# Optimization experiments

Measured on AMD Instinct MI355X. Metric: run time of the kernel, lower is better.

Reference implementation:

```python
import jax, jax.numpy as jnp
import numpy as np

EPS = 1e-12  # torch F.normalize clamp_min eps


def _linear_interp(t, M):
    # PyTorch F.interpolate(mode='linear', align_corners=False) along last axis.
    L = t.shape[-1]
    src = (jnp.arange(M, dtype=t.dtype) + 0.5) * (L / M) - 0.5
    src = jnp.maximum(src, 0.0)
    i0 = jnp.minimum(jnp.floor(src).astype(jnp.int32), L - 1)
    i1 = jnp.minimum(i0 + 1, L - 1)
    frac = src - i0.astype(t.dtype)
    return t[..., i0] * (1.0 - frac) + t[..., i1] * frac


def _l2norm(t):
    n = jnp.linalg.norm(t, axis=-1, keepdims=True)
    return t / jnp.maximum(n, EPS)


def setup_inputs() -> dict:
    key = jax.random.key(0)
    ks = jax.random.split(key, 6)
    b, dim, m = 4, 512, 4096
    h = w = 64
    heads = 8
    s = 0.02
    return {
        "x": jax.random.normal(ks[0], (b, dim, m), dtype=jnp.float32),
        "y": jax.random.normal(ks[1], (b, dim, h, w), dtype=jnp.float32),
        "temperature": jnp.ones((heads, 1, 1), dtype=jnp.float32),
        "w_kv": jax.random.normal(ks[2], (2 * dim, dim), dtype=jnp.float32) * s,
        "w_q": jax.random.normal(ks[3], (dim, dim), dtype=jnp.float32) * s,
        "w_dw": jax.random.normal(ks[4], (dim, dim, 3, 3), dtype=jnp.float32) * s,
        "w_out": jax.random.normal(ks[5], (dim, dim), dtype=jnp.float32) * s,
    }


def reference(x, y, temperature, w_kv, w_q, w_dw, w_out):
    b, c, m = x.shape
    heads = temperature.shape[0]
    hd = c // heads

    # kv = Conv1d(dim, 2*dim, k=1)(x); split into k, v
    kv = jnp.einsum('bcm,oc->bom', x, w_kv)
    k, v = jnp.split(kv, 2, axis=1)

    # q = dwconv3x3(Conv2d 1x1(y)) -> flatten -> linear-resize to m
    q = jnp.einsum('bchw,oc->bohw', y, w_q)
    q = jax.lax.conv_general_dilated(
        q, w_dw, window_strides=(1, 1), padding=[(1, 1), (1, 1)],
        dimension_numbers=('NCHW', 'OIHW', 'NCHW'))
    q = q.reshape(b, c, -1)
    q = _linear_interp(q, m)

    # split heads: [b, head, c', m]
    q = _l2norm(q.reshape(b, heads, hd, m))
    k = _l2norm(k.reshape(b, heads, hd, m))
    v = v.reshape(b, heads, hd, m)

    # channel-wise attention: [b, head, c', c']
    attn = jnp.einsum('bhcm,bhdm->bhcd', q, k) * temperature
    attn = jax.nn.softmax(attn, axis=-1)
    out = jnp.einsum('bhcd,bhdm->bhcm', attn, v).reshape(b, c, m)

    # project_out: Conv1d k=1
    return jnp.einsum('bcm,oc->bom', out, w_out)
```

## Files before the change

### kernel.cpp

```cpp
#include <hip/hip_runtime.h>
#include <hip/hip_bf16.h>
#include <math.h>

typedef float f32x4 __attribute__((ext_vector_type(4)));
typedef int   i32x4 __attribute__((ext_vector_type(4)));
typedef short s16x8 __attribute__((ext_vector_type(8)));

#define NB 4
#define NC 512
#define NM 4096
#define NHEADS 8

#define GLDS16(src, dst) __builtin_amdgcn_global_load_lds( \
    (const __attribute__((address_space(1))) void*)(src),  \
    (__attribute__((address_space(3))) void*)(dst), 16, 0, 0)

__global__ __launch_bounds__(256) void prep(
    const float* __restrict__ wdw, const float* __restrict__ wkv,
    const float* __restrict__ wq,
    __hip_bfloat16* __restrict__ Wr, __hip_bfloat16* __restrict__ wkvB,
    __hip_bfloat16* __restrict__ wqT, __hip_bfloat16* __restrict__ zeropad,
    float* __restrict__ norms)
{
  long idx = (long)blockIdx.x * 256 + threadIdx.x;
  if (idx < 2359296) {
    int r = (int)(idx / 262144);
    int rem = (int)(idx % 262144);
    int o = rem >> 9, i = rem & 511;
    Wr[idx] = __float2bfloat16(wdw[((long)o * 512 + i) * 9 + r]);
  } else if (idx < 2883584) {
    long j = idx - 2359296;
    wkvB[j] = __float2bfloat16(wkv[j]);
  } else if (idx < 3145728) {
    long j = idx - 2883584;
    int c = (int)(j >> 9), cp = (int)(j & 511);
    wqT[j] = __float2bfloat16(wq[(long)cp * 512 + c]);
  } else if (idx < 3145856) {
    zeropad[idx - 3145728] = __float2bfloat16(0.f);
  } else if (idx < 3149952) {
    norms[idx - 3145856] = 0.f;
  }
}

__global__ __launch_bounds__(256) void transpose_k(
    const float* __restrict__ x, const float* __restrict__ y,
    __hip_bfloat16* __restrict__ xT, __hip_bfloat16* __restrict__ yT)
{
  __shared__ __hip_bfloat16 tile[64][68];
  int z = blockIdx.z;
  const float* src = ((z < 4) ? x : y) + (long)(z & 3) * ((long)NC * NM);
  __hip_bfloat16* dst = (z < 4 ? xT : yT) + (long)(z & 3) * ((long)NC * NM);
  int tm = blockIdx.x * 64, tc = blockIdx.y * 64;
  int tx4 = threadIdx.x & 15, trow = threadIdx.x >> 4;
  #pragma unroll
  for (int p = 0; p < 4; p++) {
    int crow = trow + p * 16;
    f32x4 v = *(const f32x4*)&src[(long)(tc + crow) * NM + tm + tx4 * 4];
    #pragma unroll
    for (int t = 0; t < 4; t++) tile[crow][tx4 * 4 + t] = __float2bfloat16(v[t]);
  }
  __syncthreads();
  #pragma unroll
  for (int p = 0; p < 4; p++) {
    int mrow = trow + p * 16;
    union { ushort4 u4; unsigned short u[4]; } o;
    #pragma unroll
    for (int t = 0; t < 4; t++)
      o.u[t] = *(const unsigned short*)&tile[tx4 * 4 + t][mrow];
    *(ushort4*)&dst[(long)(tm + mrow) * NC + tc + tx4 * 4] = o.u4;
  }
}

__global__ __launch_bounds__(256) void gemm_bt(
    const __hip_bfloat16* __restrict__ Aall, long sA,
    const __hip_bfloat16* __restrict__ Ball, long sB,
    __hip_bfloat16* __restrict__ Cball, float* __restrict__ Cfall, long sC,
    int M, int N, int Kd, int outMode)
{
  const __hip_bfloat16* A = Aall + (long)blockIdx.z * sA;
  const __hip_bfloat16* B = Ball + (long)blockIdx.z * sB;
  const int m0 = blockIdx.y * 128, n0 = blockIdx.x * 128;
  __shared__ __hip_bfloat16 As[128 * 32];
  __shared__ __hip_bfloat16 Bs[128 * 32];
  const int tid = threadIdx.x;
  const int wid = tid >> 6, lane = tid & 63;
  const int wm = (wid >> 1) * 64, wn = (wid & 1) * 64;
  const int quad = lane >> 4, l16 = lane & 15;
  const int srow = wid * 32 + (lane >> 2);
  const int scol = (lane & 3) * 8;
  f32x4 acc[4][4] = {};
  for (int k0 = 0; k0 < Kd; k0 += 32) {
    __syncthreads();
    #pragma unroll
    for (int t = 0; t < 2; t++) {
      GLDS16(A + (long)(m0 + srow + t * 16) * Kd + k0 + scol,
             As + (wid * 32 + t * 16) * 32);
      GLDS16(B + (long)(n0 + srow + t * 16) * Kd + k0 + scol,
             Bs + (wid * 32 + t * 16) * 32);
    }
    __builtin_amdgcn_s_waitcnt(0);
    __syncthreads();
    s16x8 bfr[4];
    #pragma unroll
    for (int j = 0; j < 4; j++)
      bfr[j] = *(const s16x8*)(&Bs[(wn + j * 16 + l16) * 32 + quad * 8]);
    #pragma unroll
    for (int i = 0; i < 4; i++) {
      s16x8 af = *(const s16x8*)(&As[(wm + i * 16 + l16) * 32 + quad * 8]);
      #pragma unroll
      for (int j = 0; j < 4; j++)
        acc[i][j] = __builtin_amdgcn_mfma_f32_16x16x32_bf16(af, bfr[j], acc[i][j], 0, 0, 0);
    }
  }
  if (outMode == 1) {
    float* C = Cfall + (long)blockIdx.z * sC;
    #pragma unroll
    for (int i = 0; i < 4; i++)
      #pragma unroll
      for (int j = 0; j < 4; j++) {
        int rbase = m0 + wm + i * 16 + quad * 4;
        int col = n0 + wn + j * 16 + l16;
        #pragma unroll
        for (int r = 0; r < 4; r++)
          C[(long)(rbase + r) * N + col] = acc[i][j][r];
      }
  } else if (outMode == 2) {
    __hip_bfloat16* C = Cball;
    const int rt = blockIdx.z;
    #pragma unroll
    for (int i = 0; i < 4; i++)
      #pragma unroll
      for (int j = 0; j < 4; j++) {
        int obase = m0 + wm + i * 16 + quad * 4;
        int col = n0 + wn + j * 16 + l16;
        #pragma unroll
        for (int r = 0; r < 4; r++) {
          int o = obase + r;
          long idx = ((((long)(rt * 32 + (o >> 4)) * 16 + (col >> 5)) << 9)
                      + ((col >> 3) & 3) * 128 + (o & 15) * 8 + (col & 7));
          C[idx] = __float2bfloat16(acc[i][j][r]);
        }
      }
  } else {
    __hip_bfloat16* C = Cball + (long)blockIdx.z * sC;
    #pragma unroll
    for (int i = 0; i < 4; i++)
      #pragma unroll
      for (int j = 0; j < 4; j++) {
        int rbase = m0 + wm + i * 16 + quad * 4;
        int col = n0 + wn + j * 16 + l16;
        #pragma unroll
        for (int r = 0; r < 4; r++)
          C[(long)(rbase + r) * N + col] = __float2bfloat16(acc[i][j][r]);
      }
  }
}

__global__ __launch_bounds__(256) void gemm_kv(
    const __hip_bfloat16* __restrict__ wkvB,
    const __hip_bfloat16* __restrict__ xT,
    __hip_bfloat16* __restrict__ Kb,
    __hip_bfloat16* __restrict__ Vt,
    float* __restrict__ knorm2)
{
  const int z = blockIdx.z;
  const int b = z & 3;
  const bool kmode = (z < 4);
  const long S = (long)NM * NC;
  const __hip_bfloat16* A = kmode ? wkvB : (xT + b * S);
  const __hip_bfloat16* B = kmode ? (xT + b * S) : (wkvB + 262144);
  __hip_bfloat16* C = kmode ? (Kb + b * S) : (Vt + b * S);
  const int m0 = (kmode ? blockIdx.y : blockIdx.x) * 128;
  const int n0 = (kmode ? blockIdx.x : blockIdx.y) * 128;
  const int N = kmode ? NM : NC;
  __shared__ __hip_bfloat16 As[128 * 32];
  __shared__ __hip_bfloat16 Bs[128 * 32];
  const int tid = threadIdx.x;
  const int wid = tid >> 6, lane = tid & 63;
  const int wm = (wid >> 1) * 64, wn = (wid & 1) * 64;
  const int quad = lane >> 4, l16 = lane & 15;
  const int srow = wid * 32 + (lane >> 2);
  const int scol = (lane & 3) * 8;
  f32x4 acc[4][4] = {};
  for (int k0 = 0; k0 < NC; k0 += 32) {
    __syncthreads();
    #pragma unroll
    for (int t = 0; t < 2; t++) {
      GLDS16(A + (long)(m0 + srow + t * 16) * NC + k0 + scol,
             As + (wid * 32 + t * 16) * 32);
      GLDS16(B + (long)(n0 + srow + t * 16) * NC + k0 + scol,
             Bs + (wid * 32 + t * 16) * 32);
    }
    __builtin_amdgcn_s_waitcnt(0);
    __syncthreads();
    s16x8 bfr[4];
    #pragma unroll
    for (int j = 0; j < 4; j++)
      bfr[j] = *(const s16x8*)(&Bs[(wn + j * 16 + l16) * 32 + quad * 8]);
    #pragma unroll
    for (int i = 0; i < 4; i++) {
      s16x8 af = *(const s16x8*)(&As[(wm + i * 16 + l16) * 32 + quad * 8]);
      #pragma unroll
      for (int j = 0; j < 4; j++)
        acc[i][j] = __builtin_amdgcn_mfma_f32_16x16x32_bf16(af, bfr[j], acc[i][j], 0, 0, 0);
    }
  }
  #pragma unroll
  for (int i = 0; i < 4; i++)
    #pragma unroll
    for (int j = 0; j < 4; j++) {
      int rbase = m0 + wm + i * 16 + quad * 4;
      int col = n0 + wn + j * 16 + l16;
      #pragma unroll
      for (int r = 0; r < 4; r++)
        C[(long)(rbase + r) * N + col] = __float2bfloat16(acc[i][j][r]);
    }
  if (kmode) {
    #pragma unroll
    for (int i = 0; i < 4; i++) {
      int rbase = m0 + wm + i * 16 + quad * 4;
      #pragma unroll
      for (int r = 0; r < 4; r++) {
        float s = 0.f;
        #pragma unroll
        for (int j = 0; j < 4; j++) s += acc[i][j][r] * acc[i][j][r];
        s += __shfl_xor(s, 1); s += __shfl_xor(s, 2);
        s += __shfl_xor(s, 4); s += __shfl_xor(s, 8);
        if (l16 == 0) atomicAdd(&knorm2[b * 512 + rbase + r], s);
      }
    }
  }
}

__global__ __launch_bounds__(256) void conv3x3(
    const __hip_bfloat16* __restrict__ Wp,
    const __hip_bfloat16* __restrict__ yT,
    const __hip_bfloat16* __restrict__ zeropad,
    __hip_bfloat16* __restrict__ q2,
    float* __restrict__ qnorm2)
{
  const int b = blockIdx.z;
  const int n0 = blockIdx.x * 128;
  const int m0 = blockIdx.y * 128;
  __shared__ __hip_bfloat16 Bs[256 * 32];
  const int tid = threadIdx.x;
  const int wid = tid >> 6, lane = tid & 63;
  const int wm = (wid >> 1) * 64, wn = (wid & 1) * 64;
  const int quad = lane >> 4, l16 = lane & 15;
  const int lrow = lane >> 2;
  const int h0 = n0 >> 6;
  const __hip_bfloat16* yb = yT + (long)b * NM * NC;
  f32x4 acc[4][4] = {};
  const s16x8 zero8 = {0, 0, 0, 0, 0, 0, 0, 0};

  const int sq = ((lane & 3) ^ ((lane >> 3) & 3)) * 8;

  const int mb0 = (m0 + wm) >> 4;
  const __hip_bfloat16* Abase = Wp + (long)lane * 8;

  int addr0[3][4];
  unsigned vbits = 0;
  #pragma unroll
  for (int t = 0; t < 3; t++) {
    #pragma unroll
    for (int j = 0; j < 4; j++) {
      int nl = wn + j * 16 + l16;
      int wq_ = nl & 63, hr = nl >> 6;
      int wp = wq_ + t - 1;
      unsigned v = ((unsigned)wp) < 64u;
      int p = v ? (hr * 64 + wp) : 0;
      addr0[t][j] = p * 32 + ((quad ^ ((p >> 1) & 3)) * 8);
      vbits |= v << (t * 4 + j);
    }
  }

  for (int icb = 0; icb < 16; icb++) {
    __syncthreads();
    #pragma unroll
    for (int t = 0; t < 4; t++) {
      int p = wid * 64 + t * 16 + lrow;
      int hw = (h0 - 1) * 64 + p;
      const __hip_bfloat16* src = (((unsigned)hw) < (unsigned)NM)
          ? (yb + (long)hw * NC + icb * 32 + sq) : zeropad;
      GLDS16(src, Bs + (wid * 64 + t * 16) * 32);
    }
    __builtin_amdgcn_s_waitcnt(0);
    __syncthreads();
    #pragma unroll
    for (int g = 0; g < 3; g++) {
      #pragma unroll
      for (int t = 0; t < 3; t++) {
        const int rt = g * 3 + t;
        s16x8 bfr[4];
        #pragma unroll
        for (int j = 0; j < 4; j++) {
          s16x8 tt = *(const s16x8*)(&Bs[addr0[t][j] + g * 2048]);
          bfr[j] = ((vbits >> (t * 4 + j)) & 1u) ? tt : zero8;
        }
        #pragma unroll
        for (int i = 0; i < 4; i++) {
          s16x8 af = *(const s16x8*)(Abase +
              ((long)((rt * 32 + mb0 + i) * 16 + icb) << 9));
          #pragma unroll
          for (int j = 0; j < 4; j++)
            acc[i][j] = __builtin_amdgcn_mfma_f32_16x16x32_bf16(af, bfr[j], acc[i][j], 0, 0, 0);
        }
      }
    }
  }
  __hip_bfloat16* Cb = q2 + (long)b * NC * NM;
  #pragma unroll
  for (int i = 0; i < 4; i++)
    #pragma unroll
    for (int j = 0; j < 4; j++) {
      int rbase = m0 + wm + i * 16 + quad * 4;
      int col = n0 + wn + j * 16 + l16;
      #pragma unroll
      for (int r = 0; r < 4; r++)
        Cb[(long)(rbase + r) * NM + col] = __float2bfloat16(acc[i][j][r]);
    }
  #pragma unroll
  for (int i = 0; i < 4; i++) {
    int rbase = m0 + wm + i * 16 + quad * 4;
    #pragma unroll
    for (int r = 0; r < 4; r++) {
      float s = 0.f;
      #pragma unroll
      for (int j = 0; j < 4; j++) s += acc[i][j][r] * acc[i][j][r];
      s += __shfl_xor(s, 1); s += __shfl_xor(s, 2);
      s += __shfl_xor(s, 4); s += __shfl_xor(s, 8);
      if (l16 == 0) atomicAdd(&qnorm2[b * 512 + rbase + r], s);
    }
  }
}

__global__ __launch_bounds__(256) void attn_g(
    const __hip_bfloat16* __restrict__ q2, const __hip_bfloat16* __restrict__ Kb,
    float* __restrict__ Gpart)
{
  const int mc = blockIdx.x, h = blockIdx.y, b = blockIdx.z;
  const __hip_bfloat16* qrow = q2 + ((long)b * NC + h * 64) * NM + mc * 512;
  const __hip_bfloat16* krow = Kb + ((long)b * NC + h * 64) * NM + mc * 512;
  __shared__ __hip_bfloat16 Qs[64 * 40];
  __shared__ __hip_bfloat16 Ks[64 * 40];
  const int tid = threadIdx.x;
  const int wid = tid >> 6, lane = tid & 63;
  const int wc = (wid >> 1) * 32, wd = (wid & 1) * 32;
  const int quad = lane >> 4, l16 = lane & 15;
  const int srow = tid >> 2, scol = (tid & 3) * 8;
  f32x4 acc[2][2] = {};
  for (int k0 = 0; k0 < 512; k0 += 32) {
    __syncthreads();
    *(i32x4*)(&Qs[srow * 40 + scol]) = *(const i32x4*)(&qrow[(long)srow * NM + k0 + scol]);
    *(i32x4*)(&Ks[srow * 40 + scol]) = *(const i32x4*)(&krow[(long)srow * NM + k0 + scol]);
    __syncthreads();
    s16x8 bfr[2];
    #pragma unroll
    for (int j = 0; j < 2; j++)
      bfr[j] = *(const s16x8*)(&Ks[(wd + j * 16 + l16) * 40 + quad * 8]);
    #pragma unroll
    for (int i = 0; i < 2; i++) {
      s16x8 af = *(const s16x8*)(&Qs[(wc + i * 16 + l16) * 40 + quad * 8]);
      #pragma unroll
      for (int j = 0; j < 2; j++)
        acc[i][j] = __builtin_amdgcn_mfma_f32_16x16x32_bf16(af, bfr[j], acc[i][j], 0, 0, 0);
    }
  }
  float* gp = Gpart + ((long)((b * 8 + h) * 8 + mc)) * 4096;
  #pragma unroll
  for (int i = 0; i < 2; i++)
    #pragma unroll
    for (int j = 0; j < 2; j++)
      #pragma unroll
      for (int r = 0; r < 4; r++)
        gp[(wc + i * 16 + quad * 4 + r) * 64 + wd + j * 16 + l16] = acc[i][j][r];
}

__global__ __launch_bounds__(256) void softmax_wa(
    const float* __restrict__ Gpart, const float* __restrict__ qnorm2,
    const float* __restrict__ knorm2, const float* __restrict__ temp,
    const float* __restrict__ wout, __hip_bfloat16* __restrict__ Wa)
{
  const int oc = blockIdx.x, h = blockIdx.y, b = blockIdx.z;
  __shared__ float G[64][64];
  __shared__ float Wt[64][65];
  const int tid = threadIdx.x;
  const float tv = temp[h];
  for (int e = tid; e < 4096; e += 256) {
    float s = 0.f;
    #pragma unroll
    for (int p = 0; p < 8; p++)
      s += Gpart[((long)((b * 8 + h) * 8 + p)) * 4096 + e];
    int c = e >> 6, d = e & 63;
    float qn = fmaxf(sqrtf(qnorm2[b * 512 + h * 64 + c]), 1e-12f);
    float kn = fmaxf(sqrtf(knorm2[b * 512 + h * 64 + d]), 1e-12f);
    G[c][d] = s * tv / (qn * kn);
    Wt[c][d] = wout[(long)(oc * 64 + c) * 512 + h * 64 + d];
  }
  __syncthreads();
  int row = tid >> 2, s4 = tid & 3;
  float mx = -1e30f;
  for (int d = s4; d < 64; d += 4) mx = fmaxf(mx, G[row][d]);
  mx = fmaxf(mx, __shfl_xor(mx, 1));
  mx = fmaxf(mx, __shfl_xor(mx, 2));
  float sum = 0.f;
  for (int d = s4; d < 64; d += 4) { float e = __expf(G[row][d] - mx); G[row][d] = e; sum += e; }
  sum += __shfl_xor(sum, 1);
  sum += __shfl_xor(sum, 2);
  float inv = 1.f / sum;
  for (int d = s4; d < 64; d += 4) G[row][d] *= inv;
  __syncthreads();
  int d = tid & 63, og = tid >> 6;
  #pragma unroll
  for (int k2 = 0; k2 < 16; k2++) {
    int o = og * 16 + k2;
    float s = 0.f;
    #pragma unroll 8
    for (int c = 0; c < 64; c++) s += Wt[o][c] * G[c][d];
    Wa[((long)b * 512 + oc * 64 + o) * 512 + h * 64 + d] = __float2bfloat16(s);
  }
}

extern "C" void kernel_launch(void* const* d_in, const int* in_sizes, int n_in,
                              void* d_out, int out_size, void* d_ws, size_t ws_size,
                              hipStream_t stream) {
  const float* x    = (const float*)d_in[0];
  const float* y    = (const float*)d_in[1];
  const float* temp = (const float*)d_in[2];
  const float* wkv  = (const float*)d_in[3];
  const float* wq   = (const float*)d_in[4];
  const float* wdw  = (const float*)d_in[5];
  const float* wout = (const float*)d_in[6];
  float* out = (float*)d_out;

  char* ws = (char*)d_ws;
  const long TEN = 16777216;
  __hip_bfloat16* xT  = (__hip_bfloat16*)(ws);
  __hip_bfloat16* q2  = xT;
  __hip_bfloat16* yT  = (__hip_bfloat16*)(ws + TEN);
  float* Gpart        = (float*)(ws + TEN);
  __hip_bfloat16* Wa  = (__hip_bfloat16*)(ws + TEN + 4718592);
  __hip_bfloat16* Kb  = (__hip_bfloat16*)(ws + 2 * TEN);
  __hip_bfloat16* Vt  = (__hip_bfloat16*)(ws + 3 * TEN);
  __hip_bfloat16* Wfold = (__hip_bfloat16*)(ws + 4 * TEN);
  __hip_bfloat16* Wr    = (__hip_bfloat16*)(ws + 4 * TEN + 4718592);
  __hip_bfloat16* wkvB  = (__hip_bfloat16*)(ws + 4 * TEN + 9437184);
  __hip_bfloat16* wqT   = (__hip_bfloat16*)(ws + 4 * TEN + 10485760);
  __hip_bfloat16* zeropad = (__hip_bfloat16*)(ws + 4 * TEN + 11010048);
  float* norms          = (float*)(ws + 4 * TEN + 11010304);
  float* knorm2 = norms;
  float* qnorm2 = norms + 2048;

  const long S = (long)4096 * 512;
  const long S2 = (long)512 * 512;
  dim3 blk(256);

  prep<<<dim3(12305), blk, 0, stream>>>(wdw, wkv, wq, Wr, wkvB, wqT, zeropad, norms);
  transpose_k<<<dim3(64, 8, 8), blk, 0, stream>>>(x, y, xT, yT);
  gemm_bt<<<dim3(4, 4, 9), blk, 0, stream>>>(Wr, S2, wqT, 0L, Wfold, nullptr, 0L, 512, 512, 512, 2);
  gemm_kv<<<dim3(32, 4, 8), blk, 0, stream>>>(wkvB, xT, Kb, Vt, knorm2);
  conv3x3<<<dim3(32, 4, 4), blk, 0, stream>>>(Wfold, yT, zeropad, q2, qnorm2);
  attn_g<<<dim3(8, 8, 4), blk, 0, stream>>>(q2, Kb, Gpart);
  softmax_wa<<<dim3(8, 8, 4), blk, 0, stream>>>(Gpart, qnorm2, knorm2, temp, wout, Wa);
  gemm_bt<<<dim3(32, 4, 4), blk, 0, stream>>>(Wa, S2, Vt, S, nullptr, out, S, 512, 4096, 512, 1);
  (void)in_sizes; (void)n_in; (void)out_size; (void)ws_size;
}
```

Before: 323.0 us.

## Double-buffer conv3x3 weight and input tiles in LDS with async prefetch

The 3x3 conv GEMM kernel now stages the weight (A) fragments through LDS instead of reading them directly from global memory on every MFMA step. Both the A and B tiles are double-buffered, and the next stage is prefetched with global_load_lds while the current stage computes. This is meant to hide global load latency and cut redundant global weight reads across waves. In exchange it uses much more LDS (about 80KB per block), which may lower occupancy, and adds a barrier per tap group.

```diff
diff --git a/kernel.cpp b/kernel.cpp
--- a/kernel.cpp
+++ b/kernel.cpp
@@ -242,21 +242,21 @@
   const int b = blockIdx.z;
   const int n0 = blockIdx.x * 128;
   const int m0 = blockIdx.y * 128;
-  __shared__ __hip_bfloat16 Bs[256 * 32];
+  __shared__ __hip_bfloat16 As2[2][24 * 512];
+  __shared__ __hip_bfloat16 Bs2[2][256 * 32];
   const int tid = threadIdx.x;
   const int wid = tid >> 6, lane = tid & 63;
   const int wm = (wid >> 1) * 64, wn = (wid & 1) * 64;
   const int quad = lane >> 4, l16 = lane & 15;
   const int lrow = lane >> 2;
   const int h0 = n0 >> 6;
+  const int mb0b = m0 >> 4;
+  const int mwl = wm >> 4;
   const __hip_bfloat16* yb = yT + (long)b * NM * NC;
   f32x4 acc[4][4] = {};
   const s16x8 zero8 = {0, 0, 0, 0, 0, 0, 0, 0};
 
   const int sq = ((lane & 3) ^ ((lane >> 3) & 3)) * 8;
-
-  const int mb0 = (m0 + wm) >> 4;
-  const __hip_bfloat16* Abase = Wp + (long)lane * 8;
 
   int addr0[3][4];
   unsigned vbits = 0;
@@ -274,40 +274,73 @@
     }
   }
 
+
+  #pragma unroll
+  for (int k = 0; k < 6; k++) {
+    int f = wid * 6 + k;
+    GLDS16(Wp + (((long)(((f >> 3)) * 32 + mb0b + (f & 7)) * 16 + 0) << 9) + lane * 8,
+           &As2[0][f * 512]);
+  }
+  #pragma unroll
+  for (int t = 0; t < 4; t++) {
+    int pr = wid * 64 + t * 16 + lrow;
+    int hw = (h0 - 1) * 64 + pr;
+    const __hip_bfloat16* src = (((unsigned)hw) < (unsigned)NM)
+        ? (yb + (long)hw * NC + sq) : zeropad;
+    GLDS16(src, &Bs2[0][(wid * 64 + t * 16) * 32]);
+  }
+  __builtin_amdgcn_s_waitcnt(0);
+  __syncthreads();
+
   for (int icb = 0; icb < 16; icb++) {
-    __syncthreads();
-    #pragma unroll
-    for (int t = 0; t < 4; t++) {
-      int p = wid * 64 + t * 16 + lrow;
-      int hw = (h0 - 1) * 64 + p;
-      const __hip_bfloat16* src = (((unsigned)hw) < (unsigned)NM)
-          ? (yb + (long)hw * NC + icb * 32 + sq) : zeropad;
-      GLDS16(src, Bs + (wid * 64 + t * 16) * 32);
-    }
-    __builtin_amdgcn_s_waitcnt(0);
-    __syncthreads();
+    const __hip_bfloat16* Bcur = &Bs2[icb & 1][0];
     #pragma unroll
     for (int g = 0; g < 3; g++) {
+      const int cb = (icb ^ g) & 1;
+      const __hip_bfloat16* Acur = &As2[cb][0];
+      __hip_bfloat16* Anxt = (__hip_bfloat16*)&As2[cb ^ 1][0];
+      if (icb < 15 || g < 2) {
+        const int gn = (g == 2) ? 0 : g + 1;
+        const int icbn = (g == 2) ? icb + 1 : icb;
+        #pragma unroll
+        for (int k = 0; k < 6; k++) {
+          int f = wid * 6 + k;
+          GLDS16(Wp + (((long)((gn * 3 + (f >> 3)) * 32 + mb0b + (f & 7)) * 16 + icbn) << 9) + lane * 8,
+                 Anxt + f * 512);
+        }
+      }
+      if (g == 1 && icb < 15) {
+        __hip_bfloat16* Bnxt = (__hip_bfloat16*)&Bs2[(icb & 1) ^ 1][0];
+        #pragma unroll
+        for (int t = 0; t < 4; t++) {
+          int pr = wid * 64 + t * 16 + lrow;
+          int hw = (h0 - 1) * 64 + pr;
+          const __hip_bfloat16* src = (((unsigned)hw) < (unsigned)NM)
+              ? (yb + (long)hw * NC + (icb + 1) * 32 + sq) : zeropad;
+          GLDS16(src, Bnxt + (wid * 64 + t * 16) * 32);
+        }
+      }
       #pragma unroll
       for (int t = 0; t < 3; t++) {
-        const int rt = g * 3 + t;
         s16x8 bfr[4];
         #pragma unroll
         for (int j = 0; j < 4; j++) {
-          s16x8 tt = *(const s16x8*)(&Bs[addr0[t][j] + g * 2048]);
+          s16x8 tt = *(const s16x8*)(&Bcur[addr0[t][j] + g * 2048]);
           bfr[j] = ((vbits >> (t * 4 + j)) & 1u) ? tt : zero8;
         }
         #pragma unroll
         for (int i = 0; i < 4; i++) {
-          s16x8 af = *(const s16x8*)(Abase +
-              ((long)((rt * 32 + mb0 + i) * 16 + icb) << 9));
+          s16x8 af = *(const s16x8*)(&Acur[(t * 8 + mwl + i) * 512 + lane * 8]);
           #pragma unroll
           for (int j = 0; j < 4; j++)
             acc[i][j] = __builtin_amdgcn_mfma_f32_16x16x32_bf16(af, bfr[j], acc[i][j], 0, 0, 0);
         }
       }
-    }
-  }
+      __builtin_amdgcn_s_waitcnt(0);
+      __syncthreads();
+    }
+  }
+
   __hip_bfloat16* Cb = q2 + (long)b * NC * NM;
   #pragma unroll
   for (int i = 0; i < 4; i++)
```

New measurement: 300.4 us. -7.0%, faster.

## Double-buffer conv3x3 LDS tiles and software-pipeline weight fragment loads

Applied to the files above, without the earlier changes.

The 3x3 conv implicit-GEMM kernel now uses two LDS buffers for the y tiles. The next input-channel block is staged asynchronously while the current one is being consumed. Weight (A) fragments are prefetched one tap ahead into alternating register sets, so global load latency overlaps with the MFMAs. This removes one barrier per iteration and exposes load latency to overlap, at the cost of double the LDS and extra registers, which may reduce occupancy.

```diff
diff --git a/kernel.cpp b/kernel.cpp
--- a/kernel.cpp
+++ b/kernel.cpp
@@ -242,21 +242,21 @@
   const int b = blockIdx.z;
   const int n0 = blockIdx.x * 128;
   const int m0 = blockIdx.y * 128;
-  __shared__ __hip_bfloat16 Bs[256 * 32];
+  __shared__ __hip_bfloat16 Bs2[2][256 * 32];
   const int tid = threadIdx.x;
   const int wid = tid >> 6, lane = tid & 63;
   const int wm = (wid >> 1) * 64, wn = (wid & 1) * 64;
   const int quad = lane >> 4, l16 = lane & 15;
   const int lrow = lane >> 2;
   const int h0 = n0 >> 6;
+  const int mb0b = m0 >> 4;
+  const int mwl = wm >> 4;
   const __hip_bfloat16* yb = yT + (long)b * NM * NC;
+  const __hip_bfloat16* Ab = Wp + (long)lane * 8;
   f32x4 acc[4][4] = {};
   const s16x8 zero8 = {0, 0, 0, 0, 0, 0, 0, 0};
 
   const int sq = ((lane & 3) ^ ((lane >> 3) & 3)) * 8;
-
-  const int mb0 = (m0 + wm) >> 4;
-  const __hip_bfloat16* Abase = Wp + (long)lane * 8;
 
   int addr0[3][4];
   unsigned vbits = 0;
@@ -274,40 +274,81 @@
     }
   }
 
-  for (int icb = 0; icb < 16; icb++) {
-    __syncthreads();
-    #pragma unroll
-    for (int t = 0; t < 4; t++) {
-      int p = wid * 64 + t * 16 + lrow;
-      int hw = (h0 - 1) * 64 + p;
-      const __hip_bfloat16* src = (((unsigned)hw) < (unsigned)NM)
-          ? (yb + (long)hw * NC + icb * 32 + sq) : zeropad;
-      GLDS16(src, Bs + (wid * 64 + t * 16) * 32);
-    }
-    __builtin_amdgcn_s_waitcnt(0);
-    __syncthreads();
-    #pragma unroll
-    for (int g = 0; g < 3; g++) {
-      #pragma unroll
-      for (int t = 0; t < 3; t++) {
-        const int rt = g * 3 + t;
-        s16x8 bfr[4];
-        #pragma unroll
-        for (int j = 0; j < 4; j++) {
-          s16x8 tt = *(const s16x8*)(&Bs[addr0[t][j] + g * 2048]);
-          bfr[j] = ((vbits >> (t * 4 + j)) & 1u) ? tt : zero8;
-        }
-        #pragma unroll
-        for (int i = 0; i < 4; i++) {
-          s16x8 af = *(const s16x8*)(Abase +
-              ((long)((rt * 32 + mb0 + i) * 16 + icb) << 9));
-          #pragma unroll
-          for (int j = 0; j < 4; j++)
-            acc[i][j] = __builtin_amdgcn_mfma_f32_16x16x32_bf16(af, bfr[j], acc[i][j], 0, 0, 0);
-        }
-      }
-    }
-  }
+  s16x8 pA0[4], pA1[4];
+
+#define LOADA(buf, icb_, rt_) { \
+  _Pragma("unroll") \
+  for (int i_ = 0; i_ < 4; i_++) \
+    buf[i_] = *(const s16x8*)(Ab + (((long)((rt_) * 32 + mb0b + mwl + i_) * 16 + (icb_)) << 9)); }
+
+#define TAPC(bufc, g_, t_) { \
+  s16x8 bfr[4]; \
+  _Pragma("unroll") \
+  for (int j_ = 0; j_ < 4; j_++) { \
+    s16x8 tt = *(const s16x8*)(&Bcur[addr0[t_][j_] + (g_) * 2048]); \
+    bfr[j_] = ((vbits >> ((t_) * 4 + j_)) & 1u) ? tt : zero8; \
+  } \
+  _Pragma("unroll") \
+  for (int i_ = 0; i_ < 4; i_++) { \
+    _Pragma("unroll") \
+    for (int j_ = 0; j_ < 4; j_++) \
+      acc[i_][j_] = __builtin_amdgcn_mfma_f32_16x16x32_bf16(bufc[i_], bfr[j_], acc[i_][j_], 0, 0, 0); \
+  } }
+
+#define STAGEB(icb_, bufidx) { \
+  _Pragma("unroll") \
+  for (int t_ = 0; t_ < 4; t_++) { \
+    int pr = wid * 64 + t_ * 16 + lrow; \
+    int hw = (h0 - 1) * 64 + pr; \
+    const __hip_bfloat16* src = (((unsigned)hw) < (unsigned)NM) \
+        ? (yb + (long)hw * NC + (icb_) * 32 + sq) : zeropad; \
+    GLDS16(src, &Bs2[bufidx][(wid * 64 + t_ * 16) * 32]); \
+  } }
+
+  STAGEB(0, 0);
+  LOADA(pA0, 0, 0);
+  __builtin_amdgcn_s_waitcnt(0);
+  __syncthreads();
+
+  for (int i2 = 0; i2 < 8; i2++) {
+    const int icb = 2 * i2;
+    {
+      const __hip_bfloat16* Bcur = &Bs2[0][0];
+      STAGEB(icb + 1, 1);
+      LOADA(pA1, icb, 1);      TAPC(pA0, 0, 0);
+      LOADA(pA0, icb, 2);      TAPC(pA1, 0, 1);
+      LOADA(pA1, icb, 3);      TAPC(pA0, 0, 2);
+      LOADA(pA0, icb, 4);      TAPC(pA1, 1, 0);
+      LOADA(pA1, icb, 5);      TAPC(pA0, 1, 1);
+      LOADA(pA0, icb, 6);      TAPC(pA1, 1, 2);
+      LOADA(pA1, icb, 7);      TAPC(pA0, 2, 0);
+      LOADA(pA0, icb, 8);      TAPC(pA1, 2, 1);
+      LOADA(pA1, icb + 1, 0);  TAPC(pA0, 2, 2);
+      __builtin_amdgcn_s_waitcnt(0);
+      __syncthreads();
+    }
+    {
+      const int icbo = icb + 1;
+      const __hip_bfloat16* Bcur = &Bs2[1][0];
+      if (icbo < 15) STAGEB(icbo + 1, 0);
+      LOADA(pA0, icbo, 1);     TAPC(pA1, 0, 0);
+      LOADA(pA1, icbo, 2);     TAPC(pA0, 0, 1);
+      LOADA(pA0, icbo, 3);     TAPC(pA1, 0, 2);
+      LOADA(pA1, icbo, 4);     TAPC(pA0, 1, 0);
+      LOADA(pA0, icbo, 5);     TAPC(pA1, 1, 1);
+      LOADA(pA1, icbo, 6);     TAPC(pA0, 1, 2);
+      LOADA(pA0, icbo, 7);     TAPC(pA1, 2, 0);
+      LOADA(pA1, icbo, 8);     TAPC(pA0, 2, 1);
+      { const int icbn = (icbo + 1 < 16) ? icbo + 1 : 15;
+        LOADA(pA0, icbn, 0); } TAPC(pA1, 2, 2);
+      __builtin_amdgcn_s_waitcnt(0);
+      __syncthreads();
+    }
+  }
+#undef LOADA
+#undef TAPC
+#undef STAGEB
+
   __hip_bfloat16* Cb = q2 + (long)b * NC * NM;
   #pragma unroll
   for (int i = 0; i < 4; i++)
```

New measurement: 389.7 us. 20.7% more time.
